# Kernel tuning notes

Measured on AMD Instinct MI355X. Metric: run time of the kernel, lower is better.

The kernel has to match this reference:

```python
import jax, jax.numpy as jnp
import numpy as np

N, P, C = 8, 256, 128


def setup_inputs() -> dict:
    key = jax.random.key(0)
    ks = jax.random.split(key, 16)
    s = lambda k, shape, fan_in: jax.random.normal(k, shape, jnp.float32) / np.sqrt(fan_in)
    return {
        "x": jax.random.normal(ks[0], (N, P, C), jnp.float32),
        "pos": jax.random.normal(ks[1], (N, P, P, 2), jnp.float32),
        # projections (no bias), stored (in, out)
        "Wq": s(ks[2], (C, C), C),
        "Wk": s(ks[3], (C, C), C),
        "Wv": s(ks[4], (C, C), C),
        # qk_mlp: Linear(C,C) -> ReLU -> Linear(C,1)
        "W1": s(ks[5], (C, C), C),
        "b1": jnp.zeros((C,), jnp.float32),
        "W2": s(ks[6], (C, 1), C),
        "b2": jnp.zeros((1,), jnp.float32),
        # pos_mlp: Linear(2,C) -> ReLU -> Linear(C,C)
        "Wp1": s(ks[7], (2, C), 2),
        "bp1": jnp.zeros((C,), jnp.float32),
        "Wp2": s(ks[8], (C, C), C),
        "bp2": jnp.zeros((C,), jnp.float32),
    }


def reference(x, pos, Wq, Wk, Wv, W1, b1, W2, b2, Wp1, bp1, Wp2, bp2):
    # x: [N,P,C], pos: [N,P,P,2]
    q = x @ Wq  # [N,P,C]
    k = x @ Wk
    v = x @ Wv
    pos_emb = jax.nn.relu(pos @ Wp1 + bp1) @ Wp2 + bp2  # [N,P,P,C]
    # diff[n,a,b,:] = q[n,b] - k[n,a] + pos_emb[n,a,b]
    diff = q[:, None, :, :] - k[:, :, None, :] + pos_emb  # [N,P,P,C]
    att = (jax.nn.relu(diff @ W1 + b1) @ W2 + b2)[..., 0]  # [N,P,P]
    att = jax.nn.softmax(att, axis=-1)
    # out[n,a] = sum_b att[n,a,b] * v[n,b]
    fuse = jnp.einsum("nab,nbc->nac", att, v)
    return x + fuse
```

## Files before the change

### kernel.cpp

```cpp
#include <hip/hip_runtime.h>
#include <hip/hip_bf16.h>

#define NB 8
#define PP 256
#define CC 128
#define XS 132

typedef __attribute__((ext_vector_type(8))) unsigned short ushort8;
typedef __bf16 bf16x8 __attribute__((ext_vector_type(8)));
typedef float float4v __attribute__((ext_vector_type(4)));

__device__ __forceinline__ float bf2f(unsigned short u) {
    union { unsigned int i; float f; } x; x.i = ((unsigned int)u) << 16; return x.f;
}
__device__ __forceinline__ unsigned short f2bf(float f) {
    union { float f; unsigned int i; } x; x.f = f;
    unsigned int r = x.i + 0x7fffu + ((x.i >> 16) & 1u);
    return (unsigned short)(r >> 16);
}
__device__ __forceinline__ unsigned int pk2(float a, float b) {
    return (unsigned int)f2bf(a) | ((unsigned int)f2bf(b) << 16);
}

__global__ __launch_bounds__(256) void stage1_kernel(
    const float* __restrict__ x, const float* __restrict__ Wq,
    const float* __restrict__ Wk, const float* __restrict__ Wv,
    const float* __restrict__ W1, const float* __restrict__ b1,
    const float* __restrict__ bp2, const float* __restrict__ Wp2,
    unsigned short* __restrict__ qwtb, float* __restrict__ kw,
    float* __restrict__ v, unsigned short* __restrict__ W21f,
    float* __restrict__ bvec)
{
    __shared__ float Wbuf[CC * CC];
    __shared__ float xs[32 * XS];
    __shared__ float tmp[32 * XS];
    const int t = threadIdx.x, bx = blockIdx.x;

    if (bx == 196) {
        if (t < 128) {
            float s = b1[t];
#pragma unroll 8
            for (int c = 0; c < CC; ++c) s = fmaf(bp2[c], W1[c * CC + t], s);
            bvec[t] = s;
        }
        return;
    }

    const int tc = t & 31, tr = t >> 5;
    const int j0 = tc * 4, r0 = tr * 4;

    if (bx < 192) {
        const int kind = bx >> 6;
        const int row0 = (bx & 63) * 32;
        const float* Wsrc = (kind == 0) ? Wq : (kind == 1) ? Wk : Wv;
#pragma unroll 8
        for (int i = 0; i < 64; ++i) Wbuf[i * 256 + t] = Wsrc[i * 256 + t];
#pragma unroll 4
        for (int i = 0; i < 16; ++i) {
            int idx = i * 256 + t; int r = idx >> 7, c = idx & 127;
            xs[r * XS + c] = x[(size_t)(row0 + r) * CC + c];
        }
        __syncthreads();
        float acc[4][4];
#pragma unroll
        for (int i = 0; i < 4; ++i)
#pragma unroll
            for (int jj = 0; jj < 4; ++jj) acc[i][jj] = 0.f;
#pragma unroll 2
        for (int c = 0; c < CC; ++c) {
            float4 w4 = *(const float4*)&Wbuf[c * CC + j0];
#pragma unroll
            for (int i = 0; i < 4; ++i) {
                float xv = xs[(r0 + i) * XS + c];
                acc[i][0] = fmaf(xv, w4.x, acc[i][0]); acc[i][1] = fmaf(xv, w4.y, acc[i][1]);
                acc[i][2] = fmaf(xv, w4.z, acc[i][2]); acc[i][3] = fmaf(xv, w4.w, acc[i][3]);
            }
        }
        if (kind == 2) {
#pragma unroll
            for (int i = 0; i < 4; ++i)
                *(float4*)&v[(size_t)(row0 + r0 + i) * CC + j0] =
                    make_float4(acc[i][0], acc[i][1], acc[i][2], acc[i][3]);
            return;
        }
#pragma unroll
        for (int i = 0; i < 4; ++i)
#pragma unroll
            for (int jj = 0; jj < 4; ++jj) tmp[(r0 + i) * XS + j0 + jj] = acc[i][jj];
        __syncthreads();
#pragma unroll 8
        for (int i = 0; i < 64; ++i) Wbuf[i * 256 + t] = W1[i * 256 + t];
        __syncthreads();
        float acc2[4][4];
#pragma unroll
        for (int i = 0; i < 4; ++i)
#pragma unroll
            for (int jj = 0; jj < 4; ++jj) acc2[i][jj] = 0.f;
#pragma unroll 2
        for (int c = 0; c < CC; ++c) {
            float4 w4 = *(const float4*)&Wbuf[c * CC + j0];
#pragma unroll
            for (int i = 0; i < 4; ++i) {
                float xv = tmp[(r0 + i) * XS + c];
                acc2[i][0] = fmaf(xv, w4.x, acc2[i][0]); acc2[i][1] = fmaf(xv, w4.y, acc2[i][1]);
                acc2[i][2] = fmaf(xv, w4.z, acc2[i][2]); acc2[i][3] = fmaf(xv, w4.w, acc2[i][3]);
            }
        }
        if (kind == 0) {
            int n = row0 >> 8, b0 = row0 & 255;
#pragma unroll
            for (int jj = 0; jj < 4; ++jj) {
                ushort4 pk;
                pk.x = f2bf(acc2[0][jj]); pk.y = f2bf(acc2[1][jj]);
                pk.z = f2bf(acc2[2][jj]); pk.w = f2bf(acc2[3][jj]);
                *(ushort4*)(qwtb + (size_t)(n * CC + j0 + jj) * PP + b0 + r0) = pk;
            }
        } else {
#pragma unroll
            for (int i = 0; i < 4; ++i)
                *(float4*)&kw[(size_t)(row0 + r0 + i) * CC + j0] =
                    make_float4(acc2[i][0], acc2[i][1], acc2[i][2], acc2[i][3]);
        }
    } else {
        const int row0 = (bx - 192) * 32;
#pragma unroll 8
        for (int i = 0; i < 64; ++i) Wbuf[i * 256 + t] = W1[i * 256 + t];
#pragma unroll 4
        for (int i = 0; i < 16; ++i) {
            int idx = i * 256 + t; int r = idx >> 7, c = idx & 127;
            xs[r * XS + c] = Wp2[(size_t)(row0 + r) * CC + c];
        }
        __syncthreads();
        float acc[4][4];
#pragma unroll
        for (int i = 0; i < 4; ++i)
#pragma unroll
            for (int jj = 0; jj < 4; ++jj) acc[i][jj] = 0.f;
#pragma unroll 2
        for (int c = 0; c < CC; ++c) {
            float4 w4 = *(const float4*)&Wbuf[c * CC + j0];
#pragma unroll
            for (int i = 0; i < 4; ++i) {
                float xv = xs[(r0 + i) * XS + c];
                acc[i][0] = fmaf(xv, w4.x, acc[i][0]); acc[i][1] = fmaf(xv, w4.y, acc[i][1]);
                acc[i][2] = fmaf(xv, w4.z, acc[i][2]); acc[i][3] = fmaf(xv, w4.w, acc[i][3]);
            }
        }
#pragma unroll
        for (int i = 0; i < 4; ++i)
#pragma unroll
            for (int jj = 0; jj < 4; ++jj) {
                int k = row0 + r0 + i, j = j0 + jj;
                int kk = k >> 5, qd = (k >> 3) & 3, e = k & 7;
                int jt = j >> 4, ln = j & 15, lane = qd * 16 + ln;
                W21f[(((kk * 8 + jt) * 64) + lane) * 8 + e] = f2bf(acc[i][jj]);
            }
    }
}

__global__ __launch_bounds__(256, 3) void attn_kernel(
    const float* __restrict__ x, const float* __restrict__ pos,
    const float* __restrict__ Wp1, const float* __restrict__ bp1,
    const float* __restrict__ W2, const float* __restrict__ b2,
    const unsigned short* __restrict__ W21f, const float* __restrict__ bvec,
    const unsigned short* __restrict__ qwtb, const float* __restrict__ kw,
    const float* __restrict__ v, float* __restrict__ out)
{
    __shared__ __attribute__((aligned(16))) unsigned short Bs[128 * 128];
    __shared__ float p0s[PP], p1s[PP];
    __shared__ float wa[CC], wb[CC], bpv[CC];
    __shared__ float logits[PP];
    __shared__ float red[8];
    __shared__ float avp[8 * 128];

    const int t = threadIdx.x;
    const int n = blockIdx.x >> 8, a = blockIdx.x & 255;
    const int lane = t & 63, wv = t >> 6;
    const int ln = lane & 15, quad = lane >> 4;

    if (t < CC) {
        wa[t]  = Wp1[t];
        wb[t]  = Wp1[CC + t];
        bpv[t] = bp1[t];
    }
    {
        const float2* pr = (const float2*)(pos + (size_t)(n * PP + a) * PP * 2);
        float2 pp = pr[t];
        p0s[t] = pp.x;
        p1s[t] = pp.y;
    }
    {
        const uint4* src = (const uint4*)W21f;
        uint4* dst = (uint4*)Bs;
#pragma unroll
        for (int i = 0; i < 8; ++i) dst[i * 256 + t] = src[i * 256 + t];
    }
    const float b2f = b2[0];

    float w2v[8], kbv[8];
    {
        const float* kwrow = kw + (size_t)(n * PP + a) * CC;
#pragma unroll
        for (int nt = 0; nt < 8; ++nt) {
            int j = nt * 16 + ln;
            w2v[nt] = W2[j];
            kbv[nt] = bvec[j] - kwrow[j];
        }
    }
    __syncthreads();

#pragma unroll 1
    for (int chunk = 0; chunk < 4; ++chunk) {
        const int rbase = chunk * 64 + wv * 16;
        const float P0 = p0s[rbase + ln];
        const float P1 = p1s[rbase + ln];

        ushort4 qv4[8];
#pragma unroll
        for (int nt = 0; nt < 8; ++nt)
            qv4[nt] = *(const ushort4*)(qwtb + (size_t)(n * CC + nt * 16 + ln) * PP
                                        + rbase + quad * 4);

        float4v acc[8];
#pragma unroll
        for (int j = 0; j < 8; ++j) acc[j] = (float4v)0.f;

#pragma unroll 1
        for (int kk = 0; kk < 4; ++kk) {
            const int ko = kk * 32 + quad * 8;
            float4 a0 = *(const float4*)&wa[ko],  a1 = *(const float4*)&wa[ko + 4];
            float4 c0 = *(const float4*)&wb[ko],  c1 = *(const float4*)&wb[ko + 4];
            float4 d0 = *(const float4*)&bpv[ko], d1 = *(const float4*)&bpv[ko + 4];
            float h0 = fmaxf(fmaf(P0, a0.x, fmaf(P1, c0.x, d0.x)), 0.f);
            float h1 = fmaxf(fmaf(P0, a0.y, fmaf(P1, c0.y, d0.y)), 0.f);
            float h2 = fmaxf(fmaf(P0, a0.z, fmaf(P1, c0.z, d0.z)), 0.f);
            float h3 = fmaxf(fmaf(P0, a0.w, fmaf(P1, c0.w, d0.w)), 0.f);
            float h4 = fmaxf(fmaf(P0, a1.x, fmaf(P1, c1.x, d1.x)), 0.f);
            float h5 = fmaxf(fmaf(P0, a1.y, fmaf(P1, c1.y, d1.y)), 0.f);
            float h6 = fmaxf(fmaf(P0, a1.z, fmaf(P1, c1.z, d1.z)), 0.f);
            float h7 = fmaxf(fmaf(P0, a1.w, fmaf(P1, c1.w, d1.w)), 0.f);
            union { bf16x8 v8; unsigned int u[4]; } cv;
            cv.u[0] = pk2(h0, h1); cv.u[1] = pk2(h2, h3);
            cv.u[2] = pk2(h4, h5); cv.u[3] = pk2(h6, h7);
            bf16x8 af = cv.v8;
#pragma unroll
            for (int j = 0; j < 8; ++j) {
                bf16x8 bfr = *(const bf16x8*)(Bs + (((kk * 8 + j) * 64) + lane) * 8);
                acc[j] = __builtin_amdgcn_mfma_f32_16x16x32_bf16(af, bfr, acc[j], 0, 0, 0);
            }
        }

        float s0 = 0.f, s1 = 0.f, s2 = 0.f, s3 = 0.f;
#pragma unroll
        for (int nt = 0; nt < 8; ++nt) {
            float kb = kbv[nt], w2 = w2v[nt];
            s0 = fmaf(fmaxf(acc[nt][0] + bf2f(qv4[nt].x) + kb, 0.f), w2, s0);
            s1 = fmaf(fmaxf(acc[nt][1] + bf2f(qv4[nt].y) + kb, 0.f), w2, s1);
            s2 = fmaf(fmaxf(acc[nt][2] + bf2f(qv4[nt].z) + kb, 0.f), w2, s2);
            s3 = fmaf(fmaxf(acc[nt][3] + bf2f(qv4[nt].w) + kb, 0.f), w2, s3);
        }
        float sr[4] = {s0, s1, s2, s3};
#pragma unroll
        for (int r = 0; r < 4; ++r) {
            float s = sr[r];
            s += __shfl_xor(s, 1);
            s += __shfl_xor(s, 2);
            s += __shfl_xor(s, 4);
            s += __shfl_xor(s, 8);
            if (ln == 0) logits[rbase + quad * 4 + r] = s + b2f;
        }
    }
    __syncthreads();

    float lv = logits[t];
    float wm = lv;
#pragma unroll
    for (int d = 1; d < 64; d <<= 1) wm = fmaxf(wm, __shfl_xor(wm, d));
    if (lane == 0) red[wv] = wm;
    __syncthreads();
    float m = fmaxf(fmaxf(red[0], red[1]), fmaxf(red[2], red[3]));
    float e = __expf(lv - m);
    float es = e;
#pragma unroll
    for (int d = 1; d < 64; d <<= 1) es += __shfl_xor(es, d);
    if (lane == 0) red[4 + wv] = es;
    __syncthreads();
    float denom = red[4] + red[5] + red[6] + red[7];
    logits[t] = e / denom;
    __syncthreads();

    {
        int c4 = (t & 31) * 4, bg = t >> 5;
        const float* vp = v + (size_t)(n * PP + bg * 32) * CC + c4;
        float4 av = make_float4(0.f, 0.f, 0.f, 0.f);
#pragma unroll 4
        for (int b = 0; b < 32; ++b) {
            float w = logits[bg * 32 + b];
            float4 vv = *(const float4*)(vp + (size_t)b * CC);
            av.x = fmaf(w, vv.x, av.x); av.y = fmaf(w, vv.y, av.y);
            av.z = fmaf(w, vv.z, av.z); av.w = fmaf(w, vv.w, av.w);
        }
        *(float4*)&avp[bg * 128 + c4] = av;
    }
    __syncthreads();
    if (t < 128) {
        int oidx = (n * PP + a) * CC + t;
        float s = x[oidx];
#pragma unroll
        for (int g = 0; g < 8; ++g) s += avp[g * 128 + t];
        out[oidx] = s;
    }
}

extern "C" void kernel_launch(void* const* d_in, const int* in_sizes, int n_in,
                              void* d_out, int out_size, void* d_ws, size_t ws_size,
                              hipStream_t stream) {
    const float* x   = (const float*)d_in[0];
    const float* pos = (const float*)d_in[1];
    const float* Wq  = (const float*)d_in[2];
    const float* Wk  = (const float*)d_in[3];
    const float* Wv  = (const float*)d_in[4];
    const float* W1  = (const float*)d_in[5];
    const float* b1  = (const float*)d_in[6];
    const float* W2  = (const float*)d_in[7];
    const float* b2  = (const float*)d_in[8];
    const float* Wp1 = (const float*)d_in[9];
    const float* bp1 = (const float*)d_in[10];
    const float* Wp2 = (const float*)d_in[11];
    const float* bp2 = (const float*)d_in[12];
    float* out = (float*)d_out;

    float* ws   = (float*)d_ws;
    float* bvec = ws;
    float* kw   = bvec + 128;
    float* v    = kw + 262144;
    unsigned short* qwtb = (unsigned short*)(v + 262144);
    unsigned short* W21f = qwtb + 262144;

    stage1_kernel<<<197, 256, 0, stream>>>(x, Wq, Wk, Wv, W1, b1, bp2, Wp2,
                                           qwtb, kw, v, W21f, bvec);
    attn_kernel<<<NB * PP, 256, 0, stream>>>(x, pos, Wp1, bp1, W2, b2,
                                             W21f, bvec, qwtb, kw, v, out);
}
```

Before: 147.6 us.

## Process two row tiles per wave to reuse B fragments, vectorize stage1 loads

The main attention kernel now gives each wave two 16-row tiles per chunk (2 chunks instead of 4). Each LDS-loaded B fragment feeds two MFMAs, halving B reads and loop overhead, and the two independent accumulator chains add instruction-level parallelism. Stage1 global-to-LDS copies and the tmp stores now use float4 accesses, and bf16 packing uses the HIP intrinsic conversion. The cost is higher register pressure from doubled accumulators and q vectors, which could lower occupancy.

```diff
diff --git a/kernel.cpp b/kernel.cpp
--- a/kernel.cpp
+++ b/kernel.cpp
@@ -6,7 +6,6 @@
 #define CC 128
 #define XS 132
 
-typedef __attribute__((ext_vector_type(8))) unsigned short ushort8;
 typedef __bf16 bf16x8 __attribute__((ext_vector_type(8)));
 typedef float float4v __attribute__((ext_vector_type(4)));
 
@@ -18,8 +17,10 @@
     unsigned int r = x.i + 0x7fffu + ((x.i >> 16) & 1u);
     return (unsigned short)(r >> 16);
 }
-__device__ __forceinline__ unsigned int pk2(float a, float b) {
-    return (unsigned int)f2bf(a) | ((unsigned int)f2bf(b) << 16);
+__device__ __forceinline__ unsigned int pkbf2(float a, float b) {
+    union { __hip_bfloat162 b2; unsigned int u; } cv;
+    cv.b2 = __float22bfloat162_rn(make_float2(a, b));
+    return cv.u;
 }
 
 __global__ __launch_bounds__(256) void stage1_kernel(
@@ -31,9 +32,9 @@
     float* __restrict__ v, unsigned short* __restrict__ W21f,
     float* __restrict__ bvec)
 {
-    __shared__ float Wbuf[CC * CC];
-    __shared__ float xs[32 * XS];
-    __shared__ float tmp[32 * XS];
+    __shared__ __attribute__((aligned(16))) float Wbuf[CC * CC];
+    __shared__ __attribute__((aligned(16))) float xs[32 * XS];
+    __shared__ __attribute__((aligned(16))) float tmp[32 * XS];
     const int t = threadIdx.x, bx = blockIdx.x;
 
     if (bx == 196) {
@@ -53,12 +54,14 @@
         const int kind = bx >> 6;
         const int row0 = (bx & 63) * 32;
         const float* Wsrc = (kind == 0) ? Wq : (kind == 1) ? Wk : Wv;
-#pragma unroll 8
-        for (int i = 0; i < 64; ++i) Wbuf[i * 256 + t] = Wsrc[i * 256 + t];
 #pragma unroll 4
-        for (int i = 0; i < 16; ++i) {
-            int idx = i * 256 + t; int r = idx >> 7, c = idx & 127;
-            xs[r * XS + c] = x[(size_t)(row0 + r) * CC + c];
+        for (int i = 0; i < 16; ++i)
+            ((float4*)Wbuf)[i * 256 + t] = ((const float4*)Wsrc)[i * 256 + t];
+#pragma unroll
+        for (int i = 0; i < 4; ++i) {
+            int idx = i * 256 + t; int r = idx >> 5, c4 = idx & 31;
+            *(float4*)&xs[r * XS + c4 * 4] =
+                ((const float4*)(x + (size_t)(row0 + r) * CC))[c4];
         }
         __syncthreads();
         float acc[4][4];
@@ -85,11 +88,12 @@
         }
 #pragma unroll
         for (int i = 0; i < 4; ++i)
-#pragma unroll
-            for (int jj = 0; jj < 4; ++jj) tmp[(r0 + i) * XS + j0 + jj] = acc[i][jj];
+            *(float4*)&tmp[(r0 + i) * XS + j0] =
+                make_float4(acc[i][0], acc[i][1], acc[i][2], acc[i][3]);
         __syncthreads();
-#pragma unroll 8
-        for (int i = 0; i < 64; ++i) Wbuf[i * 256 + t] = W1[i * 256 + t];
+#pragma unroll 4
+        for (int i = 0; i < 16; ++i)
+            ((float4*)Wbuf)[i * 256 + t] = ((const float4*)W1)[i * 256 + t];
         __syncthreads();
         float acc2[4][4];
 #pragma unroll
@@ -123,12 +127,14 @@
         }
     } else {
         const int row0 = (bx - 192) * 32;
-#pragma unroll 8
-        for (int i = 0; i < 64; ++i) Wbuf[i * 256 + t] = W1[i * 256 + t];
 #pragma unroll 4
-        for (int i = 0; i < 16; ++i) {
-            int idx = i * 256 + t; int r = idx >> 7, c = idx & 127;
-            xs[r * XS + c] = Wp2[(size_t)(row0 + r) * CC + c];
+        for (int i = 0; i < 16; ++i)
+            ((float4*)Wbuf)[i * 256 + t] = ((const float4*)W1)[i * 256 + t];
+#pragma unroll
+        for (int i = 0; i < 4; ++i) {
+            int idx = i * 256 + t; int r = idx >> 5, c4 = idx & 31;
+            *(float4*)&xs[r * XS + c4 * 4] =
+                ((const float4*)(Wp2 + (size_t)(row0 + r) * CC))[c4];
         }
         __syncthreads();
         float acc[4][4];
@@ -210,20 +216,28 @@
     __syncthreads();
 
 #pragma unroll 1
-    for (int chunk = 0; chunk < 4; ++chunk) {
-        const int rbase = chunk * 64 + wv * 16;
-        const float P0 = p0s[rbase + ln];
-        const float P1 = p1s[rbase + ln];
-
-        ushort4 qv4[8];
-#pragma unroll
-        for (int nt = 0; nt < 8; ++nt)
-            qv4[nt] = *(const ushort4*)(qwtb + (size_t)(n * CC + nt * 16 + ln) * PP
-                                        + rbase + quad * 4);
-
-        float4v acc[8];
-#pragma unroll
-        for (int j = 0; j < 8; ++j) acc[j] = (float4v)0.f;
+    for (int chunk = 0; chunk < 2; ++chunk) {
+        const int rbase = chunk * 128 + wv * 32;
+        float P0[2], P1[2];
+#pragma unroll
+        for (int i = 0; i < 2; ++i) {
+            P0[i] = p0s[rbase + i * 16 + ln];
+            P1[i] = p1s[rbase + i * 16 + ln];
+        }
+
+        ushort4 qv4[2][8];
+#pragma unroll
+        for (int i = 0; i < 2; ++i)
+#pragma unroll
+            for (int nt = 0; nt < 8; ++nt)
+                qv4[i][nt] = *(const ushort4*)(qwtb + (size_t)(n * CC + nt * 16 + ln) * PP
+                                               + rbase + i * 16 + quad * 4);
+
+        float4v acc[2][8];
+#pragma unroll
+        for (int i = 0; i < 2; ++i)
+#pragma unroll
+            for (int j = 0; j < 8; ++j) acc[i][j] = (float4v)0.f;
 
 #pragma unroll 1
         for (int kk = 0; kk < 4; ++kk) {
@@ -231,43 +245,64 @@
             float4 a0 = *(const float4*)&wa[ko],  a1 = *(const float4*)&wa[ko + 4];
             float4 c0 = *(const float4*)&wb[ko],  c1 = *(const float4*)&wb[ko + 4];
             float4 d0 = *(const float4*)&bpv[ko], d1 = *(const float4*)&bpv[ko + 4];
-            float h0 = fmaxf(fmaf(P0, a0.x, fmaf(P1, c0.x, d0.x)), 0.f);
-            float h1 = fmaxf(fmaf(P0, a0.y, fmaf(P1, c0.y, d0.y)), 0.f);
-            float h2 = fmaxf(fmaf(P0, a0.z, fmaf(P1, c0.z, d0.z)), 0.f);
-            float h3 = fmaxf(fmaf(P0, a0.w, fmaf(P1, c0.w, d0.w)), 0.f);
-            float h4 = fmaxf(fmaf(P0, a1.x, fmaf(P1, c1.x, d1.x)), 0.f);
-            float h5 = fmaxf(fmaf(P0, a1.y, fmaf(P1, c1.y, d1.y)), 0.f);
-            float h6 = fmaxf(fmaf(P0, a1.z, fmaf(P1, c1.z, d1.z)), 0.f);
-            float h7 = fmaxf(fmaf(P0, a1.w, fmaf(P1, c1.w, d1.w)), 0.f);
-            union { bf16x8 v8; unsigned int u[4]; } cv;
-            cv.u[0] = pk2(h0, h1); cv.u[1] = pk2(h2, h3);
-            cv.u[2] = pk2(h4, h5); cv.u[3] = pk2(h6, h7);
-            bf16x8 af = cv.v8;
+            bf16x8 af0, af1;
+            {
+                float h0 = fmaxf(fmaf(P0[0], a0.x, fmaf(P1[0], c0.x, d0.x)), 0.f);
+                float h1 = fmaxf(fmaf(P0[0], a0.y, fmaf(P1[0], c0.y, d0.y)), 0.f);
+                float h2 = fmaxf(fmaf(P0[0], a0.z, fmaf(P1[0], c0.z, d0.z)), 0.f);
+                float h3 = fmaxf(fmaf(P0[0], a0.w, fmaf(P1[0], c0.w, d0.w)), 0.f);
+                float h4 = fmaxf(fmaf(P0[0], a1.x, fmaf(P1[0], c1.x, d1.x)), 0.f);
+                float h5 = fmaxf(fmaf(P0[0], a1.y, fmaf(P1[0], c1.y, d1.y)), 0.f);
+                float h6 = fmaxf(fmaf(P0[0], a1.z, fmaf(P1[0], c1.z, d1.z)), 0.f);
+                float h7 = fmaxf(fmaf(P0[0], a1.w, fmaf(P1[0], c1.w, d1.w)), 0.f);
+                union { bf16x8 v8; unsigned int u[4]; } cv;
+                cv.u[0] = pkbf2(h0, h1); cv.u[1] = pkbf2(h2, h3);
+                cv.u[2] = pkbf2(h4, h5); cv.u[3] = pkbf2(h6, h7);
+                af0 = cv.v8;
+            }
+            {
+                float h0 = fmaxf(fmaf(P0[1], a0.x, fmaf(P1[1], c0.x, d0.x)), 0.f);
+                float h1 = fmaxf(fmaf(P0[1], a0.y, fmaf(P1[1], c0.y, d0.y)), 0.f);
+                float h2 = fmaxf(fmaf(P0[1], a0.z, fmaf(P1[1], c0.z, d0.z)), 0.f);
+                float h3 = fmaxf(fmaf(P0[1], a0.w, fmaf(P1[1], c0.w, d0.w)), 0.f);
+                float h4 = fmaxf(fmaf(P0[1], a1.x, fmaf(P1[1], c1.x, d1.x)), 0.f);
+                float h5 = fmaxf(fmaf(P0[1], a1.y, fmaf(P1[1], c1.y, d1.y)), 0.f);
+                float h6 = fmaxf(fmaf(P0[1], a1.z, fmaf(P1[1], c1.z, d1.z)), 0.f);
+                float h7 = fmaxf(fmaf(P0[1], a1.w, fmaf(P1[1], c1.w, d1.w)), 0.f);
+                union { bf16x8 v8; unsigned int u[4]; } cv;
+                cv.u[0] = pkbf2(h0, h1); cv.u[1] = pkbf2(h2, h3);
+                cv.u[2] = pkbf2(h4, h5); cv.u[3] = pkbf2(h6, h7);
+                af1 = cv.v8;
+            }
 #pragma unroll
             for (int j = 0; j < 8; ++j) {
                 bf16x8 bfr = *(const bf16x8*)(Bs + (((kk * 8 + j) * 64) + lane) * 8);
-                acc[j] = __builtin_amdgcn_mfma_f32_16x16x32_bf16(af, bfr, acc[j], 0, 0, 0);
-            }
-        }
-
-        float s0 = 0.f, s1 = 0.f, s2 = 0.f, s3 = 0.f;
-#pragma unroll
-        for (int nt = 0; nt < 8; ++nt) {
-            float kb = kbv[nt], w2 = w2v[nt];
-            s0 = fmaf(fmaxf(acc[nt][0] + bf2f(qv4[nt].x) + kb, 0.f), w2, s0);
-            s1 = fmaf(fmaxf(acc[nt][1] + bf2f(qv4[nt].y) + kb, 0.f), w2, s1);
-            s2 = fmaf(fmaxf(acc[nt][2] + bf2f(qv4[nt].z) + kb, 0.f), w2, s2);
-            s3 = fmaf(fmaxf(acc[nt][3] + bf2f(qv4[nt].w) + kb, 0.f), w2, s3);
-        }
-        float sr[4] = {s0, s1, s2, s3};
-#pragma unroll
-        for (int r = 0; r < 4; ++r) {
-            float s = sr[r];
-            s += __shfl_xor(s, 1);
-            s += __shfl_xor(s, 2);
-            s += __shfl_xor(s, 4);
-            s += __shfl_xor(s, 8);
-            if (ln == 0) logits[rbase + quad * 4 + r] = s + b2f;
+                acc[0][j] = __builtin_amdgcn_mfma_f32_16x16x32_bf16(af0, bfr, acc[0][j], 0, 0, 0);
+                acc[1][j] = __builtin_amdgcn_mfma_f32_16x16x32_bf16(af1, bfr, acc[1][j], 0, 0, 0);
+            }
+        }
+
+#pragma unroll
+        for (int i = 0; i < 2; ++i) {
+            float s0 = 0.f, s1 = 0.f, s2 = 0.f, s3 = 0.f;
+#pragma unroll
+            for (int nt = 0; nt < 8; ++nt) {
+                float kb = kbv[nt], w2 = w2v[nt];
+                s0 = fmaf(fmaxf(acc[i][nt][0] + bf2f(qv4[i][nt].x) + kb, 0.f), w2, s0);
+                s1 = fmaf(fmaxf(acc[i][nt][1] + bf2f(qv4[i][nt].y) + kb, 0.f), w2, s1);
+                s2 = fmaf(fmaxf(acc[i][nt][2] + bf2f(qv4[i][nt].z) + kb, 0.f), w2, s2);
+                s3 = fmaf(fmaxf(acc[i][nt][3] + bf2f(qv4[i][nt].w) + kb, 0.f), w2, s3);
+            }
+            float sr[4] = {s0, s1, s2, s3};
+#pragma unroll
+            for (int r = 0; r < 4; ++r) {
+                float s = sr[r];
+                s += __shfl_xor(s, 1);
+                s += __shfl_xor(s, 2);
+                s += __shfl_xor(s, 4);
+                s += __shfl_xor(s, 8);
+                if (ln == 0) logits[rbase + i * 16 + quad * 4 + r] = s + b2f;
+            }
         }
     }
     __syncthreads();
```

After: 158.4 us. 1.07x slower.
